# Optimization experiments

Measured on AMD Instinct MI355X. Metric: run time of the kernel, lower is better.

The kernel has to match this reference:

```python
import jax, jax.numpy as jnp
import numpy as np

RADIUS = 2
K = 2 * RADIUS + 1          # kernel_size
NP = K ** 3                  # n_patches = 125
GAMMA_W = 3.3257199          # scipy.stats.t.ppf(1 - 0.005/2, df=8+8-2)
SIGMA_INV = jnp.array([0.1, 0.1, 0.1, 50., 50., 50., 10., 10., 10.], dtype=jnp.float32)


def _shift(x):
    """x: (C,H,W,T) -> (C, K^3, H, W, T): all neighbors within radius, zero-padded borders.
    Equivalent to Tile(pad=radius) + extract_patches_3ds(valid) + combine."""
    C, H, W, T = x.shape
    xp = jnp.pad(x, ((0, 0), (RADIUS, RADIUS), (RADIUS, RADIUS), (RADIUS, RADIUS)))
    sl = [xp[:, i:i + H, j:j + W, k:k + T]
          for i in range(K) for j in range(K) for k in range(K)]
    return jnp.stack(sl, axis=1)


def _compute_w(ei, ej, vi, vj):
    """Optimal weight w_ij (StatDenoiser.compute_w)."""
    d2 = (ei - ej) ** 2
    num = 2.0 * d2 + vi + vj
    den = 2.0 * (d2 + vi + vj)
    # den==0 implies num==0 (all terms nonneg) -> w = 0.5
    w = jnp.where(den == 0, 0.5, num / jnp.where(den == 0, 1.0, den))
    var_zero = (vi == 0) | (vj == 0)
    w = jnp.where(var_zero & (ei != ej), 1.0, w)
    return w


def _t_statistic(w):
    """t = sqrt(1/(2(1-w)) - 1), inf at w==1 (StatDenoiser.compute_t_statistic)."""
    w_safe = jnp.minimum(w, 1.0 - 1e-7)
    t = jnp.sqrt(jnp.maximum(1.0 / (2.0 * (1.0 - w_safe)) - 1.0, 0.0))
    return jnp.where(w >= 1.0, jnp.inf, t)


def setup_inputs() -> dict:
    key = jax.random.key(0)
    k1, k2, k3, k4 = jax.random.split(key, 4)
    noisy = jax.random.uniform(k1, (3, 128, 128, 4), dtype=jnp.float32)
    guidance = jax.random.normal(k2, (9, 128, 128, 4), dtype=jnp.float32)
    estimands = jax.random.uniform(k3, (3, 128, 128, 4), dtype=jnp.float32)
    estimands_variance = jax.random.uniform(k4, (3, 128, 128, 4), dtype=jnp.float32)
    return {"noisy": noisy, "guidance": guidance,
            "estimands": estimands, "estimands_variance": estimands_variance}


def reference(noisy, guidance, estimands, estimands_variance):
    # ---- bilateral weights from guidance (compute_bilateral_weights) ----
    sg = _shift(guidance)                                  # (9, P, H, W, T)
    diff2 = (sg - guidance[:, None]) ** 2                  # center patch == guidance itself
    bw = jnp.exp(-0.5 * jnp.einsum('c,cphwt->phwt', SIGMA_INV, diff2))  # (P,H,W,T)

    # ---- statistical membership (compute_membership) ----
    se = _shift(estimands)                                 # (3, P, H, W, T)
    sv = _shift(estimands_variance)
    ei = estimands[:, None]                                # center estimand
    vi = estimands_variance[:, None]
    w_ij = _compute_w(ei, se, vi, sv)                      # (3, P, H, W, T)
    t = _t_statistic(w_ij)
    membership = jnp.all(t <= GAMMA_W, axis=0).astype(noisy.dtype)      # (P,H,W,T)

    # ---- combine: normalized weighted average of neighbor radiance ----
    fw = bw * membership                                   # (P,H,W,T)
    sn = _shift(noisy)                                     # (3, P, H, W, T)
    out = jnp.einsum('phwt,cphwt->chwt', fw, sn) / jnp.maximum(fw.sum(axis=0), 1e-12)
    return out
```

## Files before the change

### kernel.cpp

```cpp
#include <hip/hip_runtime.h>

typedef float v2f __attribute__((ext_vector_type(2)));

namespace {

constexpr int H = 128, W = 128, NPIX = H * W;
constexpr double GAMMA_Wd = 3.3257199;
constexpr float GAM2 = (float)(GAMMA_Wd * GAMMA_Wd);
constexpr float VBIG  = 1e30f;
constexpr float NHUGE = -1e38f;

constexpr int TR = 4, TC = 16;
constexpr int HR = TR + 4, HC = TC + 4;
constexpr int NSITE = HR * HC;
constexpr int NK = 18;
constexpr int KP = 19;
constexpr int NTHR = 512;

__global__ __launch_bounds__(NTHR)
__attribute__((amdgpu_waves_per_eu(2, 8)))
void statden(const float4* __restrict__ noisy,
             const float4* __restrict__ guid,
             const float4* __restrict__ est,
             const float4* __restrict__ var,
             float4* __restrict__ out)
{
    __shared__ float4 halo[NSITE * KP];

    const int tid   = threadIdx.x;
    const int tiler = blockIdx.x >> 3;
    const int tilec = blockIdx.x & 7;
    const int r0 = tiler * TR - 2;
    const int c0 = tilec * TC - 2;

    for (int u = tid; u < NSITE * NK; u += NTHR) {
        const int k    = u / NSITE;
        const int site = u - k * NSITE;
        const int sr  = site / HC;
        const int scp = site - sr * HC;
        const int gr = r0 + sr;
        const int gc = c0 + scp;
        const bool varslot = (k >= 12) && (k < 15);
        float4 v;
        if (((unsigned)gr < (unsigned)H) && ((unsigned)gc < (unsigned)W)) {
            const int gpix = (gr << 7) + gc;
            if (k < 9) {
                const float sca = (k < 3) ? 0.22360679774997896f
                                : (k < 6) ? 5.0f
                                          : 2.2360679774997896f;
                const float4 g = guid[k * NPIX + gpix];
                v = make_float4(g.x * sca, g.y * sca, g.z * sca, g.w * sca);
            } else if (k < 12) {
                v = est[(k - 9) * NPIX + gpix];
            } else if (k < 15) {
                const float4 w4 = var[(k - 12) * NPIX + gpix];
                v.x = (w4.x == 0.f) ? -VBIG : GAM2 * w4.x;
                v.y = (w4.y == 0.f) ? -VBIG : GAM2 * w4.y;
                v.z = (w4.z == 0.f) ? -VBIG : GAM2 * w4.z;
                v.w = (w4.w == 0.f) ? -VBIG : GAM2 * w4.w;
            } else {
                v = noisy[(k - 15) * NPIX + gpix];
            }
        } else {
            const float pad = varslot ? -VBIG : 0.f;
            v = make_float4(pad, pad, pad, pad);
        }
        halo[site * KP + k] = v;
    }
    __syncthreads();

    const int p  = tid & 63;
    const int s  = tid >> 6;
    const int pr = p >> 4;
    const int pc = p & 15;

    const float4* cs = &halo[((pr + 2) * HC + (pc + 2)) * KP];

    v2f gcc[9][2];
    v2f nqc[2] = {{0.f, 0.f}, {0.f, 0.f}};
#pragma unroll
    for (int c = 0; c < 9; ++c) {
        const float4 g = cs[c];
        gcc[c][0] = (v2f){g.x, g.y};
        gcc[c][1] = (v2f){g.z, g.w};
        nqc[0] -= gcc[c][0] * gcc[c][0];
        nqc[1] -= gcc[c][1] * gcc[c][1];
    }
    v2f eiP[3][2], viP[3][2];
#pragma unroll
    for (int c = 0; c < 3; ++c) {
        const float4 e = cs[9 + c];
        eiP[c][0] = (v2f){e.x, e.y}; eiP[c][1] = (v2f){e.z, e.w};
        const float4 w4 = cs[12 + c];
        viP[c][0] = (v2f){w4.x, w4.y}; viP[c][1] = (v2f){w4.z, w4.w};
    }

    v2f accP[3][2] = {};
    v2f denP[2] = {};

#pragma unroll
    for (int cc = 0; cc < 4; ++cc) {
        const int col = s + (cc << 3);
        if (col < 25) {
            const int di = col / 5 - 2;
            const int dj = col - (col / 5) * 5 - 2;
            const float4* js = &halo[((pr + 2 + di) * HC + (pc + 2 + dj)) * KP];

            v2f qj2[2] = {};
            v2f cr[4][2] = {};
#pragma unroll
            for (int c = 0; c < 9; ++c) {
                const float4 g = js[c];
                const v2f g01 = (v2f){g.x, g.y}, g23 = (v2f){g.z, g.w};
                qj2[0] += g01 * g01;  qj2[1] += g23 * g23;
                cr[0][0] += gcc[c][0] * g.x;  cr[0][1] += gcc[c][1] * g.x;
                cr[1][0] += gcc[c][0] * g.y;  cr[1][1] += gcc[c][1] * g.y;
                cr[2][0] += gcc[c][0] * g.z;  cr[2][1] += gcc[c][1] * g.z;
                cr[3][0] += gcc[c][0] * g.w;  cr[3][1] += gcc[c][1] * g.w;
            }

            v2f rm[4][2];
#pragma unroll
            for (int c = 0; c < 3; ++c) {
                const float4 e4 = js[9 + c];
                const float4 w4 = js[12 + c];
                const float ejs[4] = {e4.x, e4.y, e4.z, e4.w};
                const float vjs[4] = {w4.x, w4.y, w4.z, w4.w};
#pragma unroll
                for (int tt = 0; tt < 4; ++tt) {
#pragma unroll
                    for (int hf = 0; hf < 2; ++hf) {
                        const v2f d  = eiP[c][hf] - ejs[tt];
                        const v2f S  = viP[c][hf] + vjs[tt];
                        const v2f dd = d * d;
                        const v2f r  = S - dd;
                        const v2f z  = dd * NHUGE;
                        const v2f rf = __builtin_elementwise_max(r, z);
                        rm[tt][hf] = (c == 0) ? rf
                                   : __builtin_elementwise_min(rm[tt][hf], rf);
                    }
                }
            }

            v2f f01[4], f23[4];
#pragma unroll
            for (int tt = 0; tt < 4; ++tt) {
                const float qjt = qj2[tt >> 1][tt & 1];
                const v2f a0 = cr[tt][0] * 2.f + (nqc[0] - qjt);
                const v2f a1 = cr[tt][1] * 2.f + (nqc[1] - qjt);
                float fv[4];
#pragma unroll
                for (int t = 0; t < 4; ++t) {
                    const bool valid = (tt - t <= 2) && (t - tt <= 2);
                    if (valid) {
                        const float av = (t < 2) ? a0[t & 1] : a1[t & 1];
                        const float rv = (t < 2) ? rm[tt][0][t & 1] : rm[tt][1][t & 1];
                        const float e  = __expf(av);
                        fv[t] = (rv >= 0.f) ? e : 0.f;
                    } else {
                        fv[t] = 0.f;
                    }
                }
                f01[tt] = (v2f){fv[0], fv[1]};
                f23[tt] = (v2f){fv[2], fv[3]};
                denP[0] += f01[tt];
                denP[1] += f23[tt];
            }
#pragma unroll
            for (int c = 0; c < 3; ++c) {
                const float4 n4 = js[15 + c];
                const float njs[4] = {n4.x, n4.y, n4.z, n4.w};
#pragma unroll
                for (int tt = 0; tt < 4; ++tt) {
                    accP[c][0] += f01[tt] * njs[tt];
                    accP[c][1] += f23[tt] * njs[tt];
                }
            }
        }
    }

    __syncthreads();
    float* red = reinterpret_cast<float*>(halo);
    {
        float* r = red + (s * 64 + p) * 17;
#pragma unroll
        for (int c = 0; c < 3; ++c) {
            r[c * 4 + 0] = accP[c][0][0]; r[c * 4 + 1] = accP[c][0][1];
            r[c * 4 + 2] = accP[c][1][0]; r[c * 4 + 3] = accP[c][1][1];
        }
        r[12] = denP[0][0]; r[13] = denP[0][1];
        r[14] = denP[1][0]; r[15] = denP[1][1];
    }
    __syncthreads();

    if (tid < 64) {
        float v[16];
        const float* rp = red + p * 17;
#pragma unroll
        for (int i = 0; i < 16; ++i) v[i] = rp[i];
#pragma unroll
        for (int k = 1; k < 8; ++k) {
            const float* rk = red + (k * 64 + p) * 17;
#pragma unroll
            for (int i = 0; i < 16; ++i) v[i] += rk[i];
        }

        const float cnt[4] = {50.f, 25.f, 25.f, 50.f};
        const float qn[4]  = {nqc[0][0], nqc[0][1], nqc[1][0], nqc[1][1]};
        const float e0[4]  = {eiP[0][0][0], eiP[0][0][1], eiP[0][1][0], eiP[0][1][1]};
        const float e1[4]  = {eiP[1][0][0], eiP[1][0][1], eiP[1][1][0], eiP[1][1][1]};
        const float e2[4]  = {eiP[2][0][0], eiP[2][0][1], eiP[2][1][0], eiP[2][1][1]};
#pragma unroll
        for (int t = 0; t < 4; ++t) {
            const bool allz = (e0[t] == 0.f) && (e1[t] == 0.f) && (e2[t] == 0.f);
            const float f0 = allz ? __expf(qn[t]) : 0.f;
            v[12 + t] += cnt[t] * f0;
        }

#pragma unroll
        for (int t = 0; t < 4; ++t) {
            const float inv = 1.f / fmaxf(v[12 + t], 1e-12f);
            v[0 + t] *= inv; v[4 + t] *= inv; v[8 + t] *= inv;
        }
        const int pid = ((tiler * TR + pr) << 7) + tilec * TC + pc;
#pragma unroll
        for (int c = 0; c < 3; ++c) {
            float4 o;
            o.x = v[c * 4 + 0]; o.y = v[c * 4 + 1];
            o.z = v[c * 4 + 2]; o.w = v[c * 4 + 3];
            out[c * NPIX + pid] = o;
        }
    }
}

}

extern "C" void kernel_launch(void* const* d_in, const int* in_sizes, int n_in,
                              void* d_out, int out_size, void* d_ws, size_t ws_size,
                              hipStream_t stream)
{
    const float4* noisy = (const float4*)d_in[0];
    const float4* guid  = (const float4*)d_in[1];
    const float4* est   = (const float4*)d_in[2];
    const float4* var   = (const float4*)d_in[3];
    float4* out = (float4*)d_out;

    statden<<<(H / TR) * (W / TC), NTHR, 0, stream>>>(noisy, guid, est, var, out);
}
```

Baseline: 15.01 us.

## Double block to 1024 threads and split neighbor columns across 16 waves

Raises the block size from 512 to 1024 threads, so each thread handles at most 2 of the 25 neighbor columns instead of 4. Center guidance values are reloaded from LDS inside the inner loop instead of being held in registers, which frees registers so the waves-per-EU hint can be raised to 4. The reduction gains a pre-stage where the upper 8 waves write partials and the lower 8 add them in before the existing 8-way reduction, at the cost of an extra barrier and more LDS reads.

```diff
diff --git a/kernel.cpp b/kernel.cpp
--- a/kernel.cpp
+++ b/kernel.cpp
@@ -15,10 +15,11 @@
 constexpr int NSITE = HR * HC;
 constexpr int NK = 18;
 constexpr int KP = 19;
-constexpr int NTHR = 512;
+constexpr int NTHR = 1024;
+
 
 __global__ __launch_bounds__(NTHR)
-__attribute__((amdgpu_waves_per_eu(2, 8)))
+__attribute__((amdgpu_waves_per_eu(4)))
 void statden(const float4* __restrict__ noisy,
              const float4* __restrict__ guid,
              const float4* __restrict__ est,
@@ -76,15 +77,13 @@
 
     const float4* cs = &halo[((pr + 2) * HC + (pc + 2)) * KP];
 
-    v2f gcc[9][2];
     v2f nqc[2] = {{0.f, 0.f}, {0.f, 0.f}};
 #pragma unroll
     for (int c = 0; c < 9; ++c) {
         const float4 g = cs[c];
-        gcc[c][0] = (v2f){g.x, g.y};
-        gcc[c][1] = (v2f){g.z, g.w};
-        nqc[0] -= gcc[c][0] * gcc[c][0];
-        nqc[1] -= gcc[c][1] * gcc[c][1];
+        const v2f g01 = (v2f){g.x, g.y}, g23 = (v2f){g.z, g.w};
+        nqc[0] -= g01 * g01;
+        nqc[1] -= g23 * g23;
     }
     v2f eiP[3][2], viP[3][2];
 #pragma unroll
@@ -99,8 +98,8 @@
     v2f denP[2] = {};
 
 #pragma unroll
-    for (int cc = 0; cc < 4; ++cc) {
-        const int col = s + (cc << 3);
+    for (int cc = 0; cc < 2; ++cc) {
+        const int col = s + (cc << 4);
         if (col < 25) {
             const int di = col / 5 - 2;
             const int dj = col - (col / 5) * 5 - 2;
@@ -110,13 +109,15 @@
             v2f cr[4][2] = {};
 #pragma unroll
             for (int c = 0; c < 9; ++c) {
-                const float4 g = js[c];
-                const v2f g01 = (v2f){g.x, g.y}, g23 = (v2f){g.z, g.w};
+                const float4 gcv = cs[c];
+                const float4 g   = js[c];
+                const v2f gc01 = (v2f){gcv.x, gcv.y}, gc23 = (v2f){gcv.z, gcv.w};
+                const v2f g01  = (v2f){g.x, g.y},     g23  = (v2f){g.z, g.w};
                 qj2[0] += g01 * g01;  qj2[1] += g23 * g23;
-                cr[0][0] += gcc[c][0] * g.x;  cr[0][1] += gcc[c][1] * g.x;
-                cr[1][0] += gcc[c][0] * g.y;  cr[1][1] += gcc[c][1] * g.y;
-                cr[2][0] += gcc[c][0] * g.z;  cr[2][1] += gcc[c][1] * g.z;
-                cr[3][0] += gcc[c][0] * g.w;  cr[3][1] += gcc[c][1] * g.w;
+                cr[0][0] += gc01 * g.x;  cr[0][1] += gc23 * g.x;
+                cr[1][0] += gc01 * g.y;  cr[1][1] += gc23 * g.y;
+                cr[2][0] += gc01 * g.z;  cr[2][1] += gc23 * g.z;
+                cr[3][0] += gc01 * g.w;  cr[3][1] += gc23 * g.w;
             }
 
             v2f rm[4][2];
@@ -181,8 +182,29 @@
 
     __syncthreads();
     float* red = reinterpret_cast<float*>(halo);
-    {
+
+    if (s >= 8) {
+        float* r = red + ((s - 8) * 64 + p) * 17;
+#pragma unroll
+        for (int c = 0; c < 3; ++c) {
+            r[c * 4 + 0] = accP[c][0][0]; r[c * 4 + 1] = accP[c][0][1];
+            r[c * 4 + 2] = accP[c][1][0]; r[c * 4 + 3] = accP[c][1][1];
+        }
+        r[12] = denP[0][0]; r[13] = denP[0][1];
+        r[14] = denP[1][0]; r[15] = denP[1][1];
+    }
+    __syncthreads();
+
+    if (s < 8) {
         float* r = red + (s * 64 + p) * 17;
+        accP[0][0][0] += r[0];  accP[0][0][1] += r[1];
+        accP[0][1][0] += r[2];  accP[0][1][1] += r[3];
+        accP[1][0][0] += r[4];  accP[1][0][1] += r[5];
+        accP[1][1][0] += r[6];  accP[1][1][1] += r[7];
+        accP[2][0][0] += r[8];  accP[2][0][1] += r[9];
+        accP[2][1][0] += r[10]; accP[2][1][1] += r[11];
+        denP[0][0] += r[12]; denP[0][1] += r[13];
+        denP[1][0] += r[14]; denP[1][1] += r[15];
 #pragma unroll
         for (int c = 0; c < 3; ++c) {
             r[c * 4 + 0] = accP[c][0][0]; r[c * 4 + 1] = accP[c][0][1];
```

Result: slower. 35.62 us (+137.3%).

## Drop shared-memory halo staging and read neighbors directly from global memory

Applied to the files above, without the earlier changes.

Replaces the cooperative LDS halo tile (4x16 pixels plus borders, 18 channels) with direct global/L2 reads of each neighbor inside the loop, using one 64-pixel row segment per block and skipping out-of-bounds neighbors instead of padding. It folds the sigma scaling and log2(e) into constants so the exponent uses exp2. The out-of-bounds zero-padding contribution is counted analytically per pixel. This removes the halo load phase and its barrier but relies on cache hits for the roughly 25x redundant neighbor reads and adds divergent branches at the borders.

```diff
diff --git a/kernel.cpp b/kernel.cpp
--- a/kernel.cpp
+++ b/kernel.cpp
@@ -10,12 +10,13 @@
 constexpr float VBIG  = 1e30f;
 constexpr float NHUGE = -1e38f;
 
-constexpr int TR = 4, TC = 16;
-constexpr int HR = TR + 4, HC = TC + 4;
-constexpr int NSITE = HR * HC;
-constexpr int NK = 18;
-constexpr int KP = 19;
+constexpr int NSL = 8;
 constexpr int NTHR = 512;
+
+constexpr double L2E2 = 0.7213475204444817;
+constexpr float SG0 = (float)(0.1 * L2E2);
+constexpr float SG1 = (float)(50.0 * L2E2);
+constexpr float SG2 = (float)(10.0 * L2E2);
 
 __global__ __launch_bounds__(NTHR)
 __attribute__((amdgpu_waves_per_eu(2, 8)))
@@ -25,162 +26,131 @@
              const float4* __restrict__ var,
              float4* __restrict__ out)
 {
-    __shared__ float4 halo[NSITE * KP];
-
-    const int tid   = threadIdx.x;
-    const int tiler = blockIdx.x >> 3;
-    const int tilec = blockIdx.x & 7;
-    const int r0 = tiler * TR - 2;
-    const int c0 = tilec * TC - 2;
-
-    for (int u = tid; u < NSITE * NK; u += NTHR) {
-        const int k    = u / NSITE;
-        const int site = u - k * NSITE;
-        const int sr  = site / HC;
-        const int scp = site - sr * HC;
-        const int gr = r0 + sr;
-        const int gc = c0 + scp;
-        const bool varslot = (k >= 12) && (k < 15);
-        float4 v;
-        if (((unsigned)gr < (unsigned)H) && ((unsigned)gc < (unsigned)W)) {
-            const int gpix = (gr << 7) + gc;
-            if (k < 9) {
-                const float sca = (k < 3) ? 0.22360679774997896f
-                                : (k < 6) ? 5.0f
-                                          : 2.2360679774997896f;
-                const float4 g = guid[k * NPIX + gpix];
-                v = make_float4(g.x * sca, g.y * sca, g.z * sca, g.w * sca);
-            } else if (k < 12) {
-                v = est[(k - 9) * NPIX + gpix];
-            } else if (k < 15) {
-                const float4 w4 = var[(k - 12) * NPIX + gpix];
-                v.x = (w4.x == 0.f) ? -VBIG : GAM2 * w4.x;
-                v.y = (w4.y == 0.f) ? -VBIG : GAM2 * w4.y;
-                v.z = (w4.z == 0.f) ? -VBIG : GAM2 * w4.z;
-                v.w = (w4.w == 0.f) ? -VBIG : GAM2 * w4.w;
-            } else {
-                v = noisy[(k - 15) * NPIX + gpix];
-            }
-        } else {
-            const float pad = varslot ? -VBIG : 0.f;
-            v = make_float4(pad, pad, pad, pad);
-        }
-        halo[site * KP + k] = v;
-    }
-    __syncthreads();
-
-    const int p  = tid & 63;
-    const int s  = tid >> 6;
-    const int pr = p >> 4;
-    const int pc = p & 15;
-
-    const float4* cs = &halo[((pr + 2) * HC + (pc + 2)) * KP];
-
-    v2f gcc[9][2];
+    __shared__ float red[NSL * 64 * 17];
+
+    const int tid = threadIdx.x;
+    const int p   = tid & 63;
+    const int s   = tid >> 6;
+    const int h   = blockIdx.x >> 1;
+    const int w   = ((blockIdx.x & 1) << 6) + p;
+    const int pid = (h << 7) + w;
+
+    const float sgl[9] = {SG0, SG0, SG0, SG1, SG1, SG1, SG2, SG2, SG2};
+
+    v2f gcd[9][2];
     v2f nqc[2] = {{0.f, 0.f}, {0.f, 0.f}};
 #pragma unroll
     for (int c = 0; c < 9; ++c) {
-        const float4 g = cs[c];
-        gcc[c][0] = (v2f){g.x, g.y};
-        gcc[c][1] = (v2f){g.z, g.w};
-        nqc[0] -= gcc[c][0] * gcc[c][0];
-        nqc[1] -= gcc[c][1] * gcc[c][1];
+        const float4 g = guid[c * NPIX + pid];
+        const v2f g01 = (v2f){g.x, g.y}, g23 = (v2f){g.z, g.w};
+        const v2f t0 = g01 * sgl[c], t1 = g23 * sgl[c];
+        nqc[0] -= t0 * g01;
+        nqc[1] -= t1 * g23;
+        gcd[c][0] = t0 * 2.f;
+        gcd[c][1] = t1 * 2.f;
     }
     v2f eiP[3][2], viP[3][2];
 #pragma unroll
     for (int c = 0; c < 3; ++c) {
-        const float4 e = cs[9 + c];
+        const float4 e = est[c * NPIX + pid];
         eiP[c][0] = (v2f){e.x, e.y}; eiP[c][1] = (v2f){e.z, e.w};
-        const float4 w4 = cs[12 + c];
-        viP[c][0] = (v2f){w4.x, w4.y}; viP[c][1] = (v2f){w4.z, w4.w};
+        const float4 vv = var[c * NPIX + pid];
+        const float v0 = (vv.x == 0.f) ? -VBIG : GAM2 * vv.x;
+        const float v1 = (vv.y == 0.f) ? -VBIG : GAM2 * vv.y;
+        const float v2 = (vv.z == 0.f) ? -VBIG : GAM2 * vv.z;
+        const float v3 = (vv.w == 0.f) ? -VBIG : GAM2 * vv.w;
+        viP[c][0] = (v2f){v0, v1}; viP[c][1] = (v2f){v2, v3};
     }
 
     v2f accP[3][2] = {};
     v2f denP[2] = {};
 
 #pragma unroll
-    for (int cc = 0; cc < 4; ++cc) {
-        const int col = s + (cc << 3);
-        if (col < 25) {
-            const int di = col / 5 - 2;
-            const int dj = col - (col / 5) * 5 - 2;
-            const float4* js = &halo[((pr + 2 + di) * HC + (pc + 2 + dj)) * KP];
-
-            v2f qj2[2] = {};
-            v2f cr[4][2] = {};
-#pragma unroll
-            for (int c = 0; c < 9; ++c) {
-                const float4 g = js[c];
-                const v2f g01 = (v2f){g.x, g.y}, g23 = (v2f){g.z, g.w};
-                qj2[0] += g01 * g01;  qj2[1] += g23 * g23;
-                cr[0][0] += gcc[c][0] * g.x;  cr[0][1] += gcc[c][1] * g.x;
-                cr[1][0] += gcc[c][0] * g.y;  cr[1][1] += gcc[c][1] * g.y;
-                cr[2][0] += gcc[c][0] * g.z;  cr[2][1] += gcc[c][1] * g.z;
-                cr[3][0] += gcc[c][0] * g.w;  cr[3][1] += gcc[c][1] * g.w;
-            }
-
-            v2f rm[4][2];
-#pragma unroll
-            for (int c = 0; c < 3; ++c) {
-                const float4 e4 = js[9 + c];
-                const float4 w4 = js[12 + c];
-                const float ejs[4] = {e4.x, e4.y, e4.z, e4.w};
-                const float vjs[4] = {w4.x, w4.y, w4.z, w4.w};
-#pragma unroll
-                for (int tt = 0; tt < 4; ++tt) {
-#pragma unroll
-                    for (int hf = 0; hf < 2; ++hf) {
-                        const v2f d  = eiP[c][hf] - ejs[tt];
-                        const v2f S  = viP[c][hf] + vjs[tt];
-                        const v2f dd = d * d;
-                        const v2f r  = S - dd;
-                        const v2f z  = dd * NHUGE;
-                        const v2f rf = __builtin_elementwise_max(r, z);
-                        rm[tt][hf] = (c == 0) ? rf
-                                   : __builtin_elementwise_min(rm[tt][hf], rf);
-                    }
+    for (int mm = 0; mm < 4; ++mm) {
+        if (mm == 3 && s != 0) continue;
+        const int col = (mm == 3) ? 24 : (s + (mm << 3));
+        const int di  = col / 5 - 2;
+        const int dj  = col - (col / 5) * 5 - 2;
+        const int hh  = h + di;
+        if ((unsigned)hh >= (unsigned)H) continue;
+        const int ww  = w + dj;
+        if ((unsigned)ww >= (unsigned)W) continue;
+        const int q = (hh << 7) + ww;
+
+        v2f qj2[2] = {};
+        v2f cr[4][2] = {};
+#pragma unroll
+        for (int c = 0; c < 9; ++c) {
+            const float4 g = guid[c * NPIX + q];
+            const v2f g01 = (v2f){g.x, g.y}, g23 = (v2f){g.z, g.w};
+            qj2[0] += (g01 * sgl[c]) * g01;
+            qj2[1] += (g23 * sgl[c]) * g23;
+            cr[0][0] += gcd[c][0] * g.x;  cr[0][1] += gcd[c][1] * g.x;
+            cr[1][0] += gcd[c][0] * g.y;  cr[1][1] += gcd[c][1] * g.y;
+            cr[2][0] += gcd[c][0] * g.z;  cr[2][1] += gcd[c][1] * g.z;
+            cr[3][0] += gcd[c][0] * g.w;  cr[3][1] += gcd[c][1] * g.w;
+        }
+
+        v2f rm[4][2];
+#pragma unroll
+        for (int c = 0; c < 3; ++c) {
+            const float4 e4 = est[c * NPIX + q];
+            const float4 w4 = var[c * NPIX + q];
+            const float ejs[4] = {e4.x, e4.y, e4.z, e4.w};
+            float vjp[4];
+            vjp[0] = (w4.x == 0.f) ? -VBIG : GAM2 * w4.x;
+            vjp[1] = (w4.y == 0.f) ? -VBIG : GAM2 * w4.y;
+            vjp[2] = (w4.z == 0.f) ? -VBIG : GAM2 * w4.z;
+            vjp[3] = (w4.w == 0.f) ? -VBIG : GAM2 * w4.w;
+#pragma unroll
+            for (int tt = 0; tt < 4; ++tt) {
+#pragma unroll
+                for (int hf = 0; hf < 2; ++hf) {
+                    const v2f d  = eiP[c][hf] - ejs[tt];
+                    const v2f S  = viP[c][hf] + vjp[tt];
+                    const v2f dd = d * d;
+                    const v2f rf = __builtin_elementwise_max(S - dd, dd * NHUGE);
+                    rm[tt][hf] = (c == 0) ? rf
+                               : __builtin_elementwise_min(rm[tt][hf], rf);
                 }
             }
-
-            v2f f01[4], f23[4];
-#pragma unroll
-            for (int tt = 0; tt < 4; ++tt) {
-                const float qjt = qj2[tt >> 1][tt & 1];
-                const v2f a0 = cr[tt][0] * 2.f + (nqc[0] - qjt);
-                const v2f a1 = cr[tt][1] * 2.f + (nqc[1] - qjt);
-                float fv[4];
-#pragma unroll
-                for (int t = 0; t < 4; ++t) {
-                    const bool valid = (tt - t <= 2) && (t - tt <= 2);
-                    if (valid) {
-                        const float av = (t < 2) ? a0[t & 1] : a1[t & 1];
-                        const float rv = (t < 2) ? rm[tt][0][t & 1] : rm[tt][1][t & 1];
-                        const float e  = __expf(av);
-                        fv[t] = (rv >= 0.f) ? e : 0.f;
-                    } else {
-                        fv[t] = 0.f;
-                    }
-                }
-                f01[tt] = (v2f){fv[0], fv[1]};
-                f23[tt] = (v2f){fv[2], fv[3]};
-                denP[0] += f01[tt];
-                denP[1] += f23[tt];
-            }
-#pragma unroll
-            for (int c = 0; c < 3; ++c) {
-                const float4 n4 = js[15 + c];
-                const float njs[4] = {n4.x, n4.y, n4.z, n4.w};
-#pragma unroll
-                for (int tt = 0; tt < 4; ++tt) {
-                    accP[c][0] += f01[tt] * njs[tt];
-                    accP[c][1] += f23[tt] * njs[tt];
+        }
+
+        v2f f01[4], f23[4];
+#pragma unroll
+        for (int tt = 0; tt < 4; ++tt) {
+            const float qjt = qj2[tt >> 1][tt & 1];
+            const v2f a0 = cr[tt][0] + (nqc[0] - qjt);
+            const v2f a1 = cr[tt][1] + (nqc[1] - qjt);
+            float fv[4];
+#pragma unroll
+            for (int t = 0; t < 4; ++t) {
+                const bool valid = (tt - t <= 2) && (t - tt <= 2);
+                if (valid) {
+                    const float av = (t < 2) ? a0[t & 1] : a1[t & 1];
+                    const float rv = (t < 2) ? rm[tt][0][t & 1] : rm[tt][1][t & 1];
+                    fv[t] = (rv >= 0.f) ? __builtin_exp2f(av) : 0.f;
+                } else {
+                    fv[t] = 0.f;
                 }
             }
-        }
-    }
-
-    __syncthreads();
-    float* red = reinterpret_cast<float*>(halo);
+            f01[tt] = (v2f){fv[0], fv[1]};
+            f23[tt] = (v2f){fv[2], fv[3]};
+            denP[0] += f01[tt];
+            denP[1] += f23[tt];
+        }
+#pragma unroll
+        for (int c = 0; c < 3; ++c) {
+            const float4 n4 = noisy[c * NPIX + q];
+            const float njs[4] = {n4.x, n4.y, n4.z, n4.w};
+#pragma unroll
+            for (int tt = 0; tt < 4; ++tt) {
+                accP[c][0] += f01[tt] * njs[tt];
+                accP[c][1] += f23[tt] * njs[tt];
+            }
+        }
+    }
+
     {
         float* r = red + (s * 64 + p) * 17;
 #pragma unroll
@@ -199,22 +169,26 @@
 #pragma unroll
         for (int i = 0; i < 16; ++i) v[i] = rp[i];
 #pragma unroll
-        for (int k = 1; k < 8; ++k) {
+        for (int k = 1; k < NSL; ++k) {
             const float* rk = red + (k * 64 + p) * 17;
 #pragma unroll
             for (int i = 0; i < 16; ++i) v[i] += rk[i];
         }
 
-        const float cnt[4] = {50.f, 25.f, 25.f, 50.f};
-        const float qn[4]  = {nqc[0][0], nqc[0][1], nqc[1][0], nqc[1][1]};
-        const float e0[4]  = {eiP[0][0][0], eiP[0][0][1], eiP[0][1][0], eiP[0][1][1]};
-        const float e1[4]  = {eiP[1][0][0], eiP[1][0][1], eiP[1][1][0], eiP[1][1][1]};
-        const float e2[4]  = {eiP[2][0][0], eiP[2][0][1], eiP[2][1][0], eiP[2][1][1]};
+        const int nh  = min(h + 2, H - 1) - max(h - 2, 0) + 1;
+        const int nw  = min(w + 2, W - 1) - max(w - 2, 0) + 1;
+        const int nhw = nh * nw;
+        const int ntt[4] = {3, 4, 4, 3};
+        const float qn[4] = {nqc[0][0], nqc[0][1], nqc[1][0], nqc[1][1]};
+        const float e0[4] = {eiP[0][0][0], eiP[0][0][1], eiP[0][1][0], eiP[0][1][1]};
+        const float e1[4] = {eiP[1][0][0], eiP[1][0][1], eiP[1][1][0], eiP[1][1][1]};
+        const float e2[4] = {eiP[2][0][0], eiP[2][0][1], eiP[2][1][0], eiP[2][1][1]};
 #pragma unroll
         for (int t = 0; t < 4; ++t) {
+            const int oob = 125 - nhw * ntt[t];
             const bool allz = (e0[t] == 0.f) && (e1[t] == 0.f) && (e2[t] == 0.f);
-            const float f0 = allz ? __expf(qn[t]) : 0.f;
-            v[12 + t] += cnt[t] * f0;
+            const float f0 = allz ? __builtin_exp2f(qn[t]) : 0.f;
+            v[12 + t] += (float)oob * f0;
         }
 
 #pragma unroll
@@ -222,7 +196,6 @@
             const float inv = 1.f / fmaxf(v[12 + t], 1e-12f);
             v[0 + t] *= inv; v[4 + t] *= inv; v[8 + t] *= inv;
         }
-        const int pid = ((tiler * TR + pr) << 7) + tilec * TC + pc;
 #pragma unroll
         for (int c = 0; c < 3; ++c) {
             float4 o;
@@ -245,5 +218,5 @@
     const float4* var   = (const float4*)d_in[3];
     float4* out = (float4*)d_out;
 
-    statden<<<(H / TR) * (W / TC), NTHR, 0, stream>>>(noisy, guid, est, var, out);
+    statden<<<NPIX / 64, NTHR, 0, stream>>>(noisy, guid, est, var, out);
 }
```

Result: no change. 15.30 us (+1.9%).
